# Kernel tuning notes

Measured on AMD Instinct MI355X. Metric: run time of the kernel, lower is better.

## Reference

```python
import jax, jax.numpy as jnp
import numpy as np

NT = 32          # nt_states
T = 64           # t_states
ST = NT + T      # total states
NEG = -1e9       # matches self.huge fill


def setup_inputs() -> dict:
    key = jax.random.key(0)
    k1, k2, k3 = jax.random.split(key, 3)
    B, n = 8, 28
    return {
        "unary_scores": jax.random.normal(k1, (B, n, T), dtype=jnp.float32),
        "rule_scores": jax.random.normal(k2, (B, NT, ST, ST), dtype=jnp.float32),
        "root_scores": jax.random.normal(k3, (B, NT), dtype=jnp.float32),
    }


def _inside(unary_scores, rule_scores, root_scores):
    # Chart indexed beta[b, width, start, state]; span (s, s+w) lives at [b, w, s].
    # Invalid (state-range) slots hold NEG, so exp() underflows them to exactly 0,
    # reproducing the terminal/nonterminal slice logic of the torch code.
    B, n, _ = unary_scores.shape
    beta = jnp.full((B, n, n, ST), NEG, dtype=unary_scores.dtype)
    beta = beta.at[:, 0, :, NT:].set(unary_scores)  # width-0 diagonal: preterminals

    mrule = rule_scores.max(axis=(2, 3))                    # [B, A]
    erule = jnp.exp(rule_scores - mrule[:, :, None, None])  # [B, A, L, R]

    for w in range(1, n):
        S = n - w                     # number of valid start positions
        k = np.arange(w)              # split offset: u = s + k
        # left child: span (s, s+k) -> width k, start s
        left = beta[:, :w, :S, :]                                  # [B, w, S, ST]
        # right child: span (s+k+1, s+w) -> width w-1-k, start s+k+1
        sr = k[:, None] + 1 + np.arange(S)[None, :]                # [w, S]
        right = beta[:, (w - 1 - k)[:, None], sr, :]               # [B, w, S, ST]

        # stable logsumexp over (k, l, r) via exp-space matmuls
        ml = left.max(-1)                                          # [B, w, S]
        mr = right.max(-1)                                         # [B, w, S]
        M = (ml + mr).max(1)                                       # [B, S]
        el = jnp.exp(left - ml[..., None])
        er = jnp.exp(right - mr[..., None] + (ml + mr - M[:, None, :])[..., None])
        numer = jnp.einsum('bksl,bksr->bslr', el, er)              # [B, S, L, R]
        total = jnp.einsum('bslr,balr->bsa', numer, erule)         # [B, S, A]
        score = jnp.log(total) + M[..., None] + mrule[:, None, :]
        beta = beta.at[:, w, :S, :NT].set(score)

    top = beta[:, n - 1, 0, :NT] + root_scores                     # span (0, n-1)
    return jax.nn.logsumexp(top, axis=1)                           # log Z, [B]


def reference(unary_scores, rule_scores, root_scores):
    return _inside(unary_scores, rule_scores, root_scores)
```

## Files before the change

kernel.cpp:

```cpp
#include <hip/hip_runtime.h>
#include <cstdint>
#include <cstddef>


#define NMAX 28
#define SLOT 17344
#define MROW 17280
#define MPROW 17312

#define O_BW1 0
#define O_BMX 960
#define O_G   1744
#define O_MSP 2528
#define O_EMR 2560
#define O_NUM 2592
#define O_RED 6160
#define O_ELT 20496
#define O_ELK 6160
#define O_ERK 14480
#define O_TRI 22800
#define LDSF  34864

__device__ __forceinline__ int off32(int w, int n) {
    return (w - 1) * n - (w * (w - 1)) / 2;
}
__device__ __forceinline__ float gload(const float* p) {
    return __hip_atomic_load(p, __ATOMIC_RELAXED, __HIP_MEMORY_SCOPE_AGENT);
}
__device__ __forceinline__ void gstore(float* p, float v) {
    __hip_atomic_store(p, v, __ATOMIC_RELAXED, __HIP_MEMORY_SCOPE_AGENT);
}
__device__ __forceinline__ unsigned gloadu(const unsigned* p) {
    return __hip_atomic_load(p, __ATOMIC_RELAXED, __HIP_MEMORY_SCOPE_AGENT);
}
__device__ __forceinline__ void gstoreu(unsigned* p, unsigned v) {
    __hip_atomic_store(p, v, __ATOMIC_RELAXED, __HIP_MEMORY_SCOPE_AGENT);
}
__device__ __forceinline__ float dot4acc(float4 m, float4 t, float acc) {
    return fmaf(m.x, t.x, fmaf(m.y, t.y, fmaf(m.z, t.z, fmaf(m.w, t.w, acc))));
}

__global__ __launch_bounds__(256) void mrule_kernel(const float* __restrict__ rule,
                                                    float* __restrict__ mrule,
                                                    unsigned* __restrict__ flags) {
    int a = blockIdx.x, b = blockIdx.y, tid = threadIdx.x;
    if (a == 0 && tid < 32)
        gstoreu(&flags[b * 32 + tid], (tid >= 16 && tid < 20) ? 2u : 0u);
    const float* base = rule + (size_t)(b * 32 + a) * 9216;
    float v = -3.0e38f;
    for (int i = tid; i < 9216; i += 256) v = fmaxf(v, base[i]);
    for (int off = 32; off > 0; off >>= 1) v = fmaxf(v, __shfl_xor(v, off, 64));
    __shared__ float red[4];
    if ((tid & 63) == 0) red[tid >> 6] = v;
    __syncthreads();
    if (tid == 0)
        mrule[b * 32 + a] = fmaxf(fmaxf(red[0], red[1]), fmaxf(red[2], red[3]));
}

__global__ __launch_bounds__(256) void pack_kernel(const float* __restrict__ rule,
                                                   const float* __restrict__ mrule,
                                                   float* __restrict__ E_TT,
                                                   float* __restrict__ E_TN,
                                                   float* __restrict__ E_NT,
                                                   float* __restrict__ E_NN) {
    int b = blockIdx.y, tid = threadIdx.x;
    int a = tid & 31;
    int cc = blockIdx.x * 8 + (tid >> 5);
    float mr = mrule[b * 32 + a];
    int l, r;
    float* dst;
    if (cc < 1024) {
        int flat = cc * 4;
        l = 32 + (flat >> 6); r = 32 + (flat & 63);
        dst = E_TT + ((size_t)(b * 1024 + cc) * 32 + a) * 4;
    } else if (cc < 1536) {
        int flat = (cc - 1024) * 4;
        l = 32 + (flat >> 5); r = flat & 31;
        dst = E_TN + ((size_t)(b * 512 + (cc - 1024)) * 32 + a) * 4;
    } else if (cc < 2048) {
        int flat = (cc - 1536) * 4;
        l = flat >> 6; r = 32 + (flat & 63);
        dst = E_NT + ((size_t)(b * 512 + (cc - 1536)) * 32 + a) * 4;
    } else {
        int flat = (cc - 2048) * 4;
        l = flat >> 5; r = flat & 31;
        dst = E_NN + ((size_t)(b * 256 + (cc - 2048)) * 32 + a) * 4;
    }
    const float4 v = *(const float4*)(rule + (((size_t)(b * 32 + a) * 96 + l) * 96 + r));
    float4 o;
    o.x = expf(v.x - mr); o.y = expf(v.y - mr);
    o.z = expf(v.z - mr); o.w = expf(v.w - mr);
    *(float4*)dst = o;
}

__device__ __forceinline__ void spin_flags(const unsigned* f, unsigned tgt, int tid) {
    if (tid < 64) {
        for (;;) {
            unsigned v = (tid < 20) ? gloadu(&f[tid]) : tgt;
            if (__ballot(v < tgt) == 0ull) break;
            __builtin_amdgcn_s_sleep(2);
        }
    }
    __syncthreads();
}

__global__ __launch_bounds__(1024, 4) void inside_kernel(
    const float* __restrict__ unary, const float* __restrict__ mrule,
    const float* __restrict__ E_TT, const float* __restrict__ E_TN,
    const float* __restrict__ E_NT, const float* __restrict__ E_NN,
    float* __restrict__ part, const float* __restrict__ root,
    float* __restrict__ out, unsigned* __restrict__ flags, int n) {
    extern __shared__ float lds[];
    const int b = blockIdx.x / 20, ch = blockIdx.x % 20;
    const int tid = threadIdx.x;
    const int a = tid & 31;
    unsigned* const myflags = flags + b * 32;
    float* const pbase = part + (size_t)(b * 4) * SLOT;

    float4 e4[2];
    {
        const float4* Eq;
        int base4;
        if (ch < 16) { Eq = (const float4*)E_TT + (size_t)b * 32768; base4 = ch * 64; }
        else         { Eq = (const float4*)E_NN + (size_t)b * 8192;  base4 = (ch - 16) * 64; }
        #pragma unroll
        for (int i = 0; i < 2; ++i)
            e4[i] = Eq[(size_t)(base4 + (tid >> 5) * 2 + i) * 32 + a];
    }
    if (tid < 32) lds[O_EMR + tid] = __expf(mrule[b * 32 + tid]);
    for (int pos = tid >> 6; pos < n; pos += 16) {
        int t = tid & 63;
        float v = unary[((size_t)b * n + pos) * 64 + t];
        float m = v;
        for (int off = 32; off > 0; off >>= 1) m = fmaxf(m, __shfl_xor(m, off, 64));
        if (t == 0) lds[O_BMX + pos] = m;
        if (ch < 16) lds[O_ELT + t * 29 + pos] = __expf(v - m);
    }
    __syncthreads();

    if (ch < 16) {
        for (int w = 1; w < n; ++w) {
            const int S = n - w;
            float* pbW = pbase + (size_t)(w & 3) * SLOT;

            if (w >= 2) {
                spin_flags(myflags, (unsigned)(w - 1), tid);
                const int wp = w - 1;
                const float* pbP = pbase + (size_t)(wp & 3) * SLOT;
                if (tid < (S + 1) * 32) {
                    int s = tid >> 5, aa = tid & 31;
                    float q[20];
                    #pragma unroll
                    for (int c = 0; c < 20; ++c) q[c] = gload(&pbP[c * 864 + tid]);
                    float tT = (((q[0] + q[1]) + (q[2] + q[3])) + ((q[4] + q[5]) + (q[6] + q[7])))
                             + (((q[8] + q[9]) + (q[10] + q[11])) + ((q[12] + q[13]) + (q[14] + q[15])));
                    float t = tT;
                    if (wp >= 3) {
                        float tN = (q[16] + q[17]) + (q[18] + q[19]);
                        float Mp = gload(&pbP[MPROW + s]);
                        t = fmaf(__expf(Mp - lds[O_MSP + s]), tN, tT);
                    }
                    float t2 = t * lds[O_EMR + aa];
                    float m2 = t2;
                    for (int off = 16; off > 0; off >>= 1)
                        m2 = fmaxf(m2, __shfl_xor(m2, off, 32));
                    lds[O_BW1 + aa * 30 + s] = t2 / m2;
                    if (aa == 0)
                        lds[O_BMX + wp * NMAX + s] = __logf(m2) + lds[O_MSP + s];
                }
                __syncthreads();
            }

            if (tid < S) {
                int s = tid;
                float M = -3.0e38f;
                for (int k = 0; k < w; ++k)
                    M = fmaxf(M, lds[O_BMX + k * NMAX + s] +
                                  lds[O_BMX + (w - 1 - k) * NMAX + s + k + 1]);
                lds[O_MSP + s] = M;
                lds[O_G + s] =
                    __expf(lds[O_BMX + s] + lds[O_BMX + (w - 1) * NMAX + s + 1] - M);
                lds[O_G + NMAX + s] =
                    __expf(lds[O_BMX + (w - 1) * NMAX + s] + lds[O_BMX + s + w] - M);
                if (ch == 0) gstore(&pbW[MROW + s], M);
            }
            __syncthreads();

            {
                const int cL = tid & 255, sh = tid >> 8;
                const bool tn = (w >= 2) && (ch < 8);
                const int cc = (w == 1) ? ch * 256 + cL
                             : (ch < 8 ? ch * 256 + cL : (ch - 8) * 256 + cL);
                int l, r;
                if (tn) { l = cc >> 5; r = cc & 31; }
                else    { l = cc >> 6; r = cc & 63; }
                unsigned short* np = (unsigned short*)(lds + O_NUM);
                for (int s = sh; s < S; s += 4) {
                    float v;
                    if (w == 1)
                        v = lds[O_ELT + l * 29 + s] * lds[O_ELT + r * 29 + (s + 1)] *
                            lds[O_G + s];
                    else if (tn)
                        v = lds[O_ELT + l * 29 + s] * lds[O_BW1 + r * 30 + (s + 1)] *
                            lds[O_G + s];
                    else
                        v = lds[O_BW1 + l * 30 + s] * lds[O_ELT + r * 29 + (s + w)] *
                            lds[O_G + NMAX + s];
                    unsigned u = __float_as_uint(v);
                    np[s * 264 + cL] = (unsigned short)((u + 0x7fffu + ((u >> 16) & 1u)) >> 16);
                }
            }
            __syncthreads();

            {
                const char* nbase = (const char*)(lds + O_NUM);
                const int g32 = tid >> 5, wv = tid >> 6;
                const bool lowhalf = (tid & 32) == 0;
                for (int s = 0; s < S; ++s) {
                    uint4 u = *(const uint4*)(nbase + s * 528 + g32 * 16);
                    float acc = 0.f;
                    #define LO(q) __uint_as_float((q) << 16)
                    #define HI(q) __uint_as_float((q) & 0xffff0000u)
                    acc = fmaf(LO(u.x), e4[0].x, acc); acc = fmaf(HI(u.x), e4[0].y, acc);
                    acc = fmaf(LO(u.y), e4[0].z, acc); acc = fmaf(HI(u.y), e4[0].w, acc);
                    acc = fmaf(LO(u.z), e4[1].x, acc); acc = fmaf(HI(u.z), e4[1].y, acc);
                    acc = fmaf(LO(u.w), e4[1].z, acc); acc = fmaf(HI(u.w), e4[1].w, acc);
                    #undef LO
                    #undef HI
                    acc += __shfl_xor(acc, 32, 64);
                    if (lowhalf) lds[O_RED + wv * 896 + s * 32 + a] = acc;
                }
            }
            __syncthreads();

            if (tid < S * 32) {
                float t = 0.f;
                #pragma unroll
                for (int g2 = 0; g2 < 16; ++g2) t += lds[O_RED + g2 * 896 + tid];
                gstore(&pbW[ch * 864 + tid], t);
            }
            __syncthreads();
            if (tid == 0) gstoreu(&myflags[ch], (unsigned)w);

            if (w == 1) {
                const float4* Eq = (ch < 8)
                    ? (const float4*)E_TN + (size_t)b * 16384 + (size_t)(ch * 64) * 32
                    : (const float4*)E_NT + (size_t)b * 16384 + (size_t)((ch - 8) * 64) * 32;
                #pragma unroll
                for (int i = 0; i < 2; ++i)
                    e4[i] = Eq[(size_t)((tid >> 5) * 2 + i) * 32 + a];
            }
        }

        if (ch == 0) {
            spin_flags(myflags, (unsigned)(n - 1), tid);
            if (tid < 32) {
                const float* pbP = pbase + (size_t)((n - 1) & 3) * SLOT;
                float q[20];
                #pragma unroll
                for (int c = 0; c < 20; ++c) q[c] = gload(&pbP[c * 864 + tid]);
                float tT = (((q[0] + q[1]) + (q[2] + q[3])) + ((q[4] + q[5]) + (q[6] + q[7])))
                         + (((q[8] + q[9]) + (q[10] + q[11])) + ((q[12] + q[13]) + (q[14] + q[15])));
                float tN = (q[16] + q[17]) + (q[18] + q[19]);
                float Mp = gload(&pbP[MPROW + 0]);
                float t = fmaf(__expf(Mp - lds[O_MSP + 0]), tN, tT);
                float v = __logf(t) + lds[O_MSP + 0] + mrule[b * 32 + tid] + root[b * 32 + tid];
                float m = v;
                for (int off = 16; off > 0; off >>= 1) m = fmaxf(m, __shfl_xor(m, off, 32));
                float e = __expf(v - m);
                for (int off = 16; off > 0; off >>= 1) e += __shfl_xor(e, off, 32);
                if (tid == 0) out[b] = m + __logf(e);
            }
        }
    } else {
        for (int w = 3; w < n; ++w) {
            const int S = n - w, Sp2 = S | 1;
            int q4 = (w - 2 + 3) >> 2; if (!(q4 & 1)) ++q4;
            const int K4 = 4 * q4;
            float* pbW = pbase + (size_t)(w & 3) * SLOT;

            spin_flags(myflags, (unsigned)(w - 2), tid);

            {
                const int wf = w - 2;
                const float* pbF = pbase + (size_t)(wf & 3) * SLOT;
                if (tid < (n - wf) * 32) {
                    int s = tid >> 5, aa = tid & 31;
                    float q[20];
                    #pragma unroll
                    for (int c = 0; c < 20; ++c) q[c] = gload(&pbF[c * 864 + tid]);
                    float tT = (((q[0] + q[1]) + (q[2] + q[3])) + ((q[4] + q[5]) + (q[6] + q[7])))
                             + (((q[8] + q[9]) + (q[10] + q[11])) + ((q[12] + q[13]) + (q[14] + q[15])));
                    float Mf = gload(&pbF[MROW + s]);
                    float t = tT;
                    if (wf >= 3) {
                        float tN = (q[16] + q[17]) + (q[18] + q[19]);
                        float Mp = gload(&pbF[MPROW + s]);
                        t = fmaf(__expf(Mp - Mf), tN, tT);
                    }
                    float t2 = t * lds[O_EMR + aa];
                    float m2 = t2;
                    for (int off = 16; off > 0; off >>= 1)
                        m2 = fmaxf(m2, __shfl_xor(m2, off, 32));
                    lds[O_TRI + (off32(wf, n) + s) * 32 + aa] = t2 / m2;
                    if (aa == 0) lds[O_BMX + wf * NMAX + s] = __logf(m2) + Mf;
                }
                __syncthreads();
            }

            if (tid < (w - 2) * 32) {
                int k = (tid >> 5) + 1, s = tid & 31;
                if (s < S) {
                    float Mp = -3.0e38f;
                    for (int k2 = 1; k2 <= w - 2; ++k2)
                        Mp = fmaxf(Mp, lds[O_BMX + k2 * NMAX + s] +
                                       lds[O_BMX + (w - 1 - k2) * NMAX + s + k2 + 1]);
                    lds[O_G + k * NMAX + s] =
                        __expf(lds[O_BMX + k * NMAX + s] +
                               lds[O_BMX + (w - 1 - k) * NMAX + s + k + 1] - Mp);
                    if (k == 1 && ch == 16) gstore(&pbW[MPROW + s], Mp);
                }
            }
            __syncthreads();

            if (tid < S * 32) {
                int s = tid >> 5, sym = tid & 31;
                int off = (sym * Sp2 + s) * K4;
                for (int kk = 1; kk <= w - 2; ++kk) {
                    lds[O_ELK + off + kk - 1] =
                        lds[O_TRI + (off32(kk, n) + s) * 32 + sym];
                    lds[O_ERK + off + kk - 1] =
                        lds[O_TRI + (off32(w - 1 - kk, n) + s + kk + 1) * 32 + sym] *
                        lds[O_G + kk * NMAX + s];
                }
                for (int k = w - 2; k < K4; ++k) {
                    lds[O_ELK + off + k] = 0.f;
                    lds[O_ERK + off + k] = 0.f;
                }
            }
            __syncthreads();

            {
                const int cL = tid & 255, sh = tid >> 8;
                const int cc = (ch - 16) * 256 + cL;
                const int l = cc >> 5, r = cc & 31;
                unsigned short* np = (unsigned short*)(lds + O_NUM);
                for (int s = sh; s < S; s += 4) {
                    const float* elp = lds + O_ELK + (l * Sp2 + s) * K4;
                    const float* erp = lds + O_ERK + (r * Sp2 + s) * K4;
                    float acc = 0.f;
                    for (int j = 0; j < K4; j += 4)
                        acc = dot4acc(*(const float4*)(elp + j),
                                      *(const float4*)(erp + j), acc);
                    unsigned u = __float_as_uint(acc);
                    np[s * 264 + cL] = (unsigned short)((u + 0x7fffu + ((u >> 16) & 1u)) >> 16);
                }
            }
            __syncthreads();

            {
                const char* nbase = (const char*)(lds + O_NUM);
                const int g32 = tid >> 5, wv = tid >> 6;
                const bool lowhalf = (tid & 32) == 0;
                for (int s = 0; s < S; ++s) {
                    uint4 u = *(const uint4*)(nbase + s * 528 + g32 * 16);
                    float acc = 0.f;
                    #define LO(q) __uint_as_float((q) << 16)
                    #define HI(q) __uint_as_float((q) & 0xffff0000u)
                    acc = fmaf(LO(u.x), e4[0].x, acc); acc = fmaf(HI(u.x), e4[0].y, acc);
                    acc = fmaf(LO(u.y), e4[0].z, acc); acc = fmaf(HI(u.y), e4[0].w, acc);
                    acc = fmaf(LO(u.z), e4[1].x, acc); acc = fmaf(HI(u.z), e4[1].y, acc);
                    acc = fmaf(LO(u.w), e4[1].z, acc); acc = fmaf(HI(u.w), e4[1].w, acc);
                    #undef LO
                    #undef HI
                    acc += __shfl_xor(acc, 32, 64);
                    if (lowhalf) lds[O_RED + wv * 896 + s * 32 + a] = acc;
                }
            }
            __syncthreads();

            if (tid < S * 32) {
                float t = 0.f;
                #pragma unroll
                for (int g2 = 0; g2 < 16; ++g2) t += lds[O_RED + g2 * 896 + tid];
                gstore(&pbW[ch * 864 + tid], t);
            }
            __syncthreads();
            if (tid == 0) gstoreu(&myflags[ch], (unsigned)w);
        }
    }
}

extern "C" void kernel_launch(void* const* d_in, const int* in_sizes, int n_in,
                              void* d_out, int out_size, void* d_ws, size_t ws_size,
                              hipStream_t stream) {
    const float* unary = (const float*)d_in[0];
    const float* rule  = (const float*)d_in[1];
    const float* root  = (const float*)d_in[2];
    float* out = (float*)d_out;

    const int B = in_sizes[2] / 32;
    int n = in_sizes[0] / (B * 64);

    float* ws = (float*)d_ws;
    float* mrule  = ws;
    float* E_TT   = mrule + (size_t)B * 32;
    float* E_TN   = E_TT + (size_t)B * 131072;
    float* E_NT   = E_TN + (size_t)B * 65536;
    float* E_NN   = E_NT + (size_t)B * 65536;
    float* part   = E_NN + (size_t)B * 32768;
    unsigned* flags = (unsigned*)(part + (size_t)B * 4 * SLOT);

    mrule_kernel<<<dim3(32, B), 256, 0, stream>>>(rule, mrule, flags);
    pack_kernel<<<dim3(288, B), 256, 0, stream>>>(rule, mrule, E_TT, E_TN, E_NT, E_NN);

    hipFuncSetAttribute((const void*)inside_kernel,
                        hipFuncAttributeMaxDynamicSharedMemorySize, LDSF * 4);

    void* args[] = {
        (void*)&unary, (void*)&mrule,
        (void*)&E_TT, (void*)&E_TN, (void*)&E_NT, (void*)&E_NN,
        (void*)&part, (void*)&root, (void*)&out, (void*)&flags, (void*)&n
    };
    hipLaunchCooperativeKernel((void*)inside_kernel, dim3(B * 20), dim3(1024),
                               args, LDSF * 4, stream);
}
```

Baseline: 242.7 us.

## Replace flag-based sync with sign-encoded data polling and fewer, wider blocks

Removes the per-chunk flag array and spin-wait barrier. Consumers now poll the partial-sum slots directly, and readiness is encoded by sign-flipping the values on alternating slot reuse, with slots pre-initialised to a negative sentinel. Per-batch blocks drop from 20 to 12, so each block covers twice the rule chunk. Partials are laid out with a 12-float pitch per (s,a) and the max values are recomputed locally instead of exchanged through global memory. This aims to cut flag round-trip latency and synchronisation cost, at the price of more work per block and correctness that relies on the sign encoding holding.

```diff
diff --git a/kernel.cpp b/kernel.cpp
--- a/kernel.cpp
+++ b/kernel.cpp
@@ -4,9 +4,8 @@
 
 
 #define NMAX 28
-#define SLOT 17344
-#define MROW 17280
-#define MPROW 17312
+#define PITCH 12
+#define SLOTF 10368
 
 #define O_BW1 0
 #define O_BMX 960
@@ -14,12 +13,12 @@
 #define O_MSP 2528
 #define O_EMR 2560
 #define O_NUM 2592
-#define O_RED 6160
-#define O_ELT 20496
-#define O_ELK 6160
-#define O_ERK 14480
-#define O_TRI 22800
-#define LDSF  34864
+#define O_RED 9612
+#define O_ELT 23948
+#define O_ELK 9612
+#define O_ERK 17932
+#define O_TRI 26252
+#define LDSF  38316
 
 __device__ __forceinline__ int off32(int w, int n) {
     return (w - 1) * n - (w * (w - 1)) / 2;
@@ -30,22 +29,13 @@
 __device__ __forceinline__ void gstore(float* p, float v) {
     __hip_atomic_store(p, v, __ATOMIC_RELAXED, __HIP_MEMORY_SCOPE_AGENT);
 }
-__device__ __forceinline__ unsigned gloadu(const unsigned* p) {
-    return __hip_atomic_load(p, __ATOMIC_RELAXED, __HIP_MEMORY_SCOPE_AGENT);
-}
-__device__ __forceinline__ void gstoreu(unsigned* p, unsigned v) {
-    __hip_atomic_store(p, v, __ATOMIC_RELAXED, __HIP_MEMORY_SCOPE_AGENT);
-}
 __device__ __forceinline__ float dot4acc(float4 m, float4 t, float acc) {
     return fmaf(m.x, t.x, fmaf(m.y, t.y, fmaf(m.z, t.z, fmaf(m.w, t.w, acc))));
 }
 
 __global__ __launch_bounds__(256) void mrule_kernel(const float* __restrict__ rule,
-                                                    float* __restrict__ mrule,
-                                                    unsigned* __restrict__ flags) {
+                                                    float* __restrict__ mrule) {
     int a = blockIdx.x, b = blockIdx.y, tid = threadIdx.x;
-    if (a == 0 && tid < 32)
-        gstoreu(&flags[b * 32 + tid], (tid >= 16 && tid < 20) ? 2u : 0u);
     const float* base = rule + (size_t)(b * 32 + a) * 9216;
     float v = -3.0e38f;
     for (int i = tid; i < 9216; i += 256) v = fmaxf(v, base[i]);
@@ -62,8 +52,14 @@
                                                    float* __restrict__ E_TT,
                                                    float* __restrict__ E_TN,
                                                    float* __restrict__ E_NT,
-                                                   float* __restrict__ E_NN) {
+                                                   float* __restrict__ E_NN,
+                                                   float* __restrict__ part) {
     int b = blockIdx.y, tid = threadIdx.x;
+    {
+        const int total = 4 * SLOTF;
+        for (int i = blockIdx.x * 256 + tid; i < total; i += 288 * 256)
+            part[(size_t)b * total + i] = -0.5f;
+    }
     int a = tid & 31;
     int cc = blockIdx.x * 8 + (tid >> 5);
     float mr = mrule[b * 32 + a];
@@ -93,15 +89,22 @@
     *(float4*)dst = o;
 }
 
-__device__ __forceinline__ void spin_flags(const unsigned* f, unsigned tgt, int tid) {
-    if (tid < 64) {
-        for (;;) {
-            unsigned v = (tid < 20) ? gloadu(&f[tid]) : tgt;
-            if (__ballot(v < tgt) == 0ull) break;
-            __builtin_amdgcn_s_sleep(2);
+__device__ __forceinline__ void poll12(const float* pp, bool oddp, int CHp,
+                                       float x[12]) {
+    for (;;) {
+        #pragma unroll
+        for (int c = 0; c < 12; ++c) x[c] = gload(pp + c);
+        if (oddp) {
+            #pragma unroll
+            for (int c = 0; c < 12; ++c) x[c] = -x[c] - 1.0f;
         }
-    }
-    __syncthreads();
+        float mn = fminf(fminf(fminf(x[0], x[1]), fminf(x[2], x[3])),
+                         fminf(fminf(x[4], x[5]), fminf(x[6], x[7])));
+        if (CHp == 12)
+            mn = fminf(mn, fminf(fminf(x[8], x[9]), fminf(x[10], x[11])));
+        if (mn >= 0.0f) break;
+        __builtin_amdgcn_s_sleep(4);
+    }
 }
 
 __global__ __launch_bounds__(1024, 4) void inside_kernel(
@@ -109,23 +112,24 @@
     const float* __restrict__ E_TT, const float* __restrict__ E_TN,
     const float* __restrict__ E_NT, const float* __restrict__ E_NN,
     float* __restrict__ part, const float* __restrict__ root,
-    float* __restrict__ out, unsigned* __restrict__ flags, int n) {
+    float* __restrict__ out, int n) {
     extern __shared__ float lds[];
-    const int b = blockIdx.x / 20, ch = blockIdx.x % 20;
+    const int b = blockIdx.x / 12, ch = blockIdx.x % 12;
     const int tid = threadIdx.x;
-    const int a = tid & 31;
-    unsigned* const myflags = flags + b * 32;
-    float* const pbase = part + (size_t)(b * 4) * SLOT;
-
-    float4 e4[2];
-    {
-        const float4* Eq;
-        int base4;
-        if (ch < 16) { Eq = (const float4*)E_TT + (size_t)b * 32768; base4 = ch * 64; }
-        else         { Eq = (const float4*)E_NN + (size_t)b * 8192;  base4 = (ch - 16) * 64; }
+    const int a = tid & 31, g = tid >> 5;
+    float* const pbase = part + (size_t)(b * 4) * SLOTF;
+
+    float4 e4[4];
+    if (ch < 8) {
+        const float4* Eq = (const float4*)E_TT + (size_t)b * 32768;
+        #pragma unroll
+        for (int i = 0; i < 4; ++i)
+            e4[i] = Eq[(size_t)(ch * 128 + g * 4 + i) * 32 + a];
+    } else {
+        const float4* Eq = (const float4*)E_NN + (size_t)b * 8192;
         #pragma unroll
         for (int i = 0; i < 2; ++i)
-            e4[i] = Eq[(size_t)(base4 + (tid >> 5) * 2 + i) * 32 + a];
+            e4[i] = Eq[(size_t)((ch - 8) * 64 + g * 2 + i) * 32 + a];
     }
     if (tid < 32) lds[O_EMR + tid] = __expf(mrule[b * 32 + tid]);
     for (int pos = tid >> 6; pos < n; pos += 16) {
@@ -134,30 +138,34 @@
         float m = v;
         for (int off = 32; off > 0; off >>= 1) m = fmaxf(m, __shfl_xor(m, off, 64));
         if (t == 0) lds[O_BMX + pos] = m;
-        if (ch < 16) lds[O_ELT + t * 29 + pos] = __expf(v - m);
+        if (ch < 8) lds[O_ELT + t * 29 + pos] = __expf(v - m);
     }
     __syncthreads();
 
-    if (ch < 16) {
+    if (ch < 8) {
         for (int w = 1; w < n; ++w) {
             const int S = n - w;
-            float* pbW = pbase + (size_t)(w & 3) * SLOT;
+            const bool oddw = ((w >> 2) & 1) != 0;
+            float* pbW = pbase + (size_t)(w & 3) * SLOTF;
 
             if (w >= 2) {
-                spin_flags(myflags, (unsigned)(w - 1), tid);
                 const int wp = w - 1;
-                const float* pbP = pbase + (size_t)(wp & 3) * SLOT;
+                const int CHp = (wp >= 3) ? 12 : 8;
+                const bool oddp = ((wp >> 2) & 1) != 0;
+                const float* pbP = pbase + (size_t)(wp & 3) * SLOTF;
                 if (tid < (S + 1) * 32) {
                     int s = tid >> 5, aa = tid & 31;
-                    float q[20];
-                    #pragma unroll
-                    for (int c = 0; c < 20; ++c) q[c] = gload(&pbP[c * 864 + tid]);
-                    float tT = (((q[0] + q[1]) + (q[2] + q[3])) + ((q[4] + q[5]) + (q[6] + q[7])))
-                             + (((q[8] + q[9]) + (q[10] + q[11])) + ((q[12] + q[13]) + (q[14] + q[15])));
+                    float Mp = -3.0e38f;
+                    for (int k = 1; k <= wp - 2; ++k)
+                        Mp = fmaxf(Mp, lds[O_BMX + k * NMAX + s] +
+                                       lds[O_BMX + (wp - 1 - k) * NMAX + s + k + 1]);
+                    float x[12];
+                    poll12(pbP + (size_t)tid * PITCH, oddp, CHp, x);
+                    float tT = (((x[0] + x[1]) + (x[2] + x[3])) +
+                                ((x[4] + x[5]) + (x[6] + x[7])));
                     float t = tT;
-                    if (wp >= 3) {
-                        float tN = (q[16] + q[17]) + (q[18] + q[19]);
-                        float Mp = gload(&pbP[MPROW + s]);
+                    if (CHp == 12) {
+                        float tN = (x[8] + x[9]) + (x[10] + x[11]);
                         t = fmaf(__expf(Mp - lds[O_MSP + s]), tN, tT);
                     }
                     float t2 = t * lds[O_EMR + aa];
@@ -168,8 +176,8 @@
                     if (aa == 0)
                         lds[O_BMX + wp * NMAX + s] = __logf(m2) + lds[O_MSP + s];
                 }
-                __syncthreads();
-            }
+            }
+            __syncthreads();
 
             if (tid < S) {
                 int s = tid;
@@ -182,20 +190,19 @@
                     __expf(lds[O_BMX + s] + lds[O_BMX + (w - 1) * NMAX + s + 1] - M);
                 lds[O_G + NMAX + s] =
                     __expf(lds[O_BMX + (w - 1) * NMAX + s] + lds[O_BMX + s + w] - M);
-                if (ch == 0) gstore(&pbW[MROW + s], M);
             }
             __syncthreads();
 
             {
-                const int cL = tid & 255, sh = tid >> 8;
-                const bool tn = (w >= 2) && (ch < 8);
-                const int cc = (w == 1) ? ch * 256 + cL
-                             : (ch < 8 ? ch * 256 + cL : (ch - 8) * 256 + cL);
+                const int cL = tid & 511, sh = tid >> 9;
+                const bool tn = (w >= 2) && (ch < 4);
+                const int cc = (w == 1) ? ch * 512 + cL
+                             : (ch < 4 ? ch * 512 + cL : (ch - 4) * 512 + cL);
                 int l, r;
                 if (tn) { l = cc >> 5; r = cc & 31; }
                 else    { l = cc >> 6; r = cc & 63; }
                 unsigned short* np = (unsigned short*)(lds + O_NUM);
-                for (int s = sh; s < S; s += 4) {
+                for (int s = sh; s < S; s += 2) {
                     float v;
                     if (w == 1)
                         v = lds[O_ELT + l * 29 + s] * lds[O_ELT + r * 29 + (s + 1)] *
@@ -207,17 +214,172 @@
                         v = lds[O_BW1 + l * 30 + s] * lds[O_ELT + r * 29 + (s + w)] *
                             lds[O_G + NMAX + s];
                     unsigned u = __float_as_uint(v);
-                    np[s * 264 + cL] = (unsigned short)((u + 0x7fffu + ((u >> 16) & 1u)) >> 16);
+                    np[s * 520 + cL] = (unsigned short)((u + 0x7fffu + ((u >> 16) & 1u)) >> 16);
                 }
             }
             __syncthreads();
 
             {
                 const char* nbase = (const char*)(lds + O_NUM);
-                const int g32 = tid >> 5, wv = tid >> 6;
+                const int wv = tid >> 6;
                 const bool lowhalf = (tid & 32) == 0;
                 for (int s = 0; s < S; ++s) {
-                    uint4 u = *(const uint4*)(nbase + s * 528 + g32 * 16);
+                    uint4 u0 = *(const uint4*)(nbase + s * 1040 + g * 32);
+                    uint4 u1 = *(const uint4*)(nbase + s * 1040 + g * 32 + 16);
+                    float acc = 0.f;
+                    #define LO(q) __uint_as_float((q) << 16)
+                    #define HI(q) __uint_as_float((q) & 0xffff0000u)
+                    acc = fmaf(LO(u0.x), e4[0].x, acc); acc = fmaf(HI(u0.x), e4[0].y, acc);
+                    acc = fmaf(LO(u0.y), e4[0].z, acc); acc = fmaf(HI(u0.y), e4[0].w, acc);
+                    acc = fmaf(LO(u0.z), e4[1].x, acc); acc = fmaf(HI(u0.z), e4[1].y, acc);
+                    acc = fmaf(LO(u0.w), e4[1].z, acc); acc = fmaf(HI(u0.w), e4[1].w, acc);
+                    acc = fmaf(LO(u1.x), e4[2].x, acc); acc = fmaf(HI(u1.x), e4[2].y, acc);
+                    acc = fmaf(LO(u1.y), e4[2].z, acc); acc = fmaf(HI(u1.y), e4[2].w, acc);
+                    acc = fmaf(LO(u1.z), e4[3].x, acc); acc = fmaf(HI(u1.z), e4[3].y, acc);
+                    acc = fmaf(LO(u1.w), e4[3].z, acc); acc = fmaf(HI(u1.w), e4[3].w, acc);
+                    #undef LO
+                    #undef HI
+                    acc += __shfl_xor(acc, 32, 64);
+                    if (lowhalf) lds[O_RED + wv * 896 + s * 32 + a] = acc;
+                }
+            }
+            __syncthreads();
+
+            if (tid < S * 32) {
+                float t = 0.f;
+                #pragma unroll
+                for (int g2 = 0; g2 < 16; ++g2) t += lds[O_RED + g2 * 896 + tid];
+                gstore(&pbW[(size_t)tid * PITCH + ch], oddw ? (-t - 1.0f) : t);
+            }
+
+            if (w == 1) {
+                const float4* Eq = (ch < 4)
+                    ? (const float4*)E_TN + (size_t)b * 16384 + (size_t)(ch * 128) * 32
+                    : (const float4*)E_NT + (size_t)b * 16384 + (size_t)((ch - 4) * 128) * 32;
+                #pragma unroll
+                for (int i = 0; i < 4; ++i)
+                    e4[i] = Eq[(size_t)(g * 4 + i) * 32 + a];
+            }
+        }
+
+        if (ch == 0 && tid < 32) {
+            const int wp = n - 1;
+            const bool oddp = ((wp >> 2) & 1) != 0;
+            const float* pbP = pbase + (size_t)(wp & 3) * SLOTF;
+            float Mp = -3.0e38f;
+            for (int k = 1; k <= wp - 2; ++k)
+                Mp = fmaxf(Mp, lds[O_BMX + k * NMAX + 0] +
+                               lds[O_BMX + (wp - 1 - k) * NMAX + k + 1]);
+            float x[12];
+            poll12(pbP + (size_t)tid * PITCH, oddp, 12, x);
+            float tT = (((x[0] + x[1]) + (x[2] + x[3])) +
+                        ((x[4] + x[5]) + (x[6] + x[7])));
+            float tN = (x[8] + x[9]) + (x[10] + x[11]);
+            float t = fmaf(__expf(Mp - lds[O_MSP + 0]), tN, tT);
+            float v = __logf(t) + lds[O_MSP + 0] + mrule[b * 32 + tid] + root[b * 32 + tid];
+            float m = v;
+            for (int off = 16; off > 0; off >>= 1) m = fmaxf(m, __shfl_xor(m, off, 32));
+            float e = __expf(v - m);
+            for (int off = 16; off > 0; off >>= 1) e += __shfl_xor(e, off, 32);
+            if (tid == 0) out[b] = m + __logf(e);
+        }
+    } else {
+        for (int w = 3; w < n; ++w) {
+            const int S = n - w, Sp2 = S | 1;
+            int q4 = (w - 2 + 3) >> 2; if (!(q4 & 1)) ++q4;
+            const int K4 = 4 * q4;
+            const bool oddw = ((w >> 2) & 1) != 0;
+            float* pbW = pbase + (size_t)(w & 3) * SLOTF;
+
+            {
+                const int wf = w - 2;
+                const int CHp = (wf >= 3) ? 12 : 8;
+                const bool oddp = ((wf >> 2) & 1) != 0;
+                const float* pbF = pbase + (size_t)(wf & 3) * SLOTF;
+                if (tid < (n - wf) * 32) {
+                    int s = tid >> 5, aa = tid & 31;
+                    float Mw = -3.0e38f;
+                    for (int k = 0; k < wf; ++k)
+                        Mw = fmaxf(Mw, lds[O_BMX + k * NMAX + s] +
+                                       lds[O_BMX + (wf - 1 - k) * NMAX + s + k + 1]);
+                    float Mp = -3.0e38f;
+                    for (int k = 1; k <= wf - 2; ++k)
+                        Mp = fmaxf(Mp, lds[O_BMX + k * NMAX + s] +
+                                       lds[O_BMX + (wf - 1 - k) * NMAX + s + k + 1]);
+                    float x[12];
+                    poll12(pbF + (size_t)tid * PITCH, oddp, CHp, x);
+                    float tT = (((x[0] + x[1]) + (x[2] + x[3])) +
+                                ((x[4] + x[5]) + (x[6] + x[7])));
+                    float t = tT;
+                    if (CHp == 12) {
+                        float tN = (x[8] + x[9]) + (x[10] + x[11]);
+                        t = fmaf(__expf(Mp - Mw), tN, tT);
+                    }
+                    float t2 = t * lds[O_EMR + aa];
+                    float m2 = t2;
+                    for (int off = 16; off > 0; off >>= 1)
+                        m2 = fmaxf(m2, __shfl_xor(m2, off, 32));
+                    lds[O_TRI + (off32(wf, n) + s) * 32 + aa] = t2 / m2;
+                    if (aa == 0) lds[O_BMX + wf * NMAX + s] = __logf(m2) + Mw;
+                }
+            }
+            __syncthreads();
+
+            if (tid < (w - 2) * 32) {
+                int k = (tid >> 5) + 1, s = tid & 31;
+                if (s < S) {
+                    float Mp = -3.0e38f;
+                    for (int k2 = 1; k2 <= w - 2; ++k2)
+                        Mp = fmaxf(Mp, lds[O_BMX + k2 * NMAX + s] +
+                                       lds[O_BMX + (w - 1 - k2) * NMAX + s + k2 + 1]);
+                    lds[O_G + k * NMAX + s] =
+                        __expf(lds[O_BMX + k * NMAX + s] +
+                               lds[O_BMX + (w - 1 - k) * NMAX + s + k + 1] - Mp);
+                }
+            }
+            __syncthreads();
+
+            if (tid < S * 32) {
+                int s = tid >> 5, sym = tid & 31;
+                int off = (sym * Sp2 + s) * K4;
+                for (int kk = 1; kk <= w - 2; ++kk) {
+                    lds[O_ELK + off + kk - 1] =
+                        lds[O_TRI + (off32(kk, n) + s) * 32 + sym];
+                    lds[O_ERK + off + kk - 1] =
+                        lds[O_TRI + (off32(w - 1 - kk, n) + s + kk + 1) * 32 + sym] *
+                        lds[O_G + kk * NMAX + s];
+                }
+                for (int k = w - 2; k < K4; ++k) {
+                    lds[O_ELK + off + k] = 0.f;
+                    lds[O_ERK + off + k] = 0.f;
+                }
+            }
+            __syncthreads();
+
+            {
+                const int cL = tid & 255, sh = tid >> 8;
+                const int cc = (ch - 8) * 256 + cL;
+                const int l = cc >> 5, r = cc & 31;
+                unsigned short* np = (unsigned short*)(lds + O_NUM);
+                for (int s = sh; s < S; s += 4) {
+                    const float* elp = lds + O_ELK + (l * Sp2 + s) * K4;
+                    const float* erp = lds + O_ERK + (r * Sp2 + s) * K4;
+                    float acc = 0.f;
+                    for (int j = 0; j < K4; j += 4)
+                        acc = dot4acc(*(const float4*)(elp + j),
+                                      *(const float4*)(erp + j), acc);
+                    unsigned u = __float_as_uint(acc);
+                    np[s * 520 + cL] = (unsigned short)((u + 0x7fffu + ((u >> 16) & 1u)) >> 16);
+                }
+            }
+            __syncthreads();
+
+            {
+                const char* nbase = (const char*)(lds + O_NUM);
+                const int wv = tid >> 6;
+                const bool lowhalf = (tid & 32) == 0;
+                for (int s = 0; s < S; ++s) {
+                    uint4 u = *(const uint4*)(nbase + s * 1040 + g * 16);
                     float acc = 0.f;
                     #define LO(q) __uint_as_float((q) << 16)
                     #define HI(q) __uint_as_float((q) & 0xffff0000u)
@@ -237,156 +399,9 @@
                 float t = 0.f;
                 #pragma unroll
                 for (int g2 = 0; g2 < 16; ++g2) t += lds[O_RED + g2 * 896 + tid];
-                gstore(&pbW[ch * 864 + tid], t);
-            }
-            __syncthreads();
-            if (tid == 0) gstoreu(&myflags[ch], (unsigned)w);
-
-            if (w == 1) {
-                const float4* Eq = (ch < 8)
-                    ? (const float4*)E_TN + (size_t)b * 16384 + (size_t)(ch * 64) * 32
-                    : (const float4*)E_NT + (size_t)b * 16384 + (size_t)((ch - 8) * 64) * 32;
-                #pragma unroll
-                for (int i = 0; i < 2; ++i)
-                    e4[i] = Eq[(size_t)((tid >> 5) * 2 + i) * 32 + a];
-            }
-        }
-
-        if (ch == 0) {
-            spin_flags(myflags, (unsigned)(n - 1), tid);
-            if (tid < 32) {
-                const float* pbP = pbase + (size_t)((n - 1) & 3) * SLOT;
-                float q[20];
-                #pragma unroll
-                for (int c = 0; c < 20; ++c) q[c] = gload(&pbP[c * 864 + tid]);
-                float tT = (((q[0] + q[1]) + (q[2] + q[3])) + ((q[4] + q[5]) + (q[6] + q[7])))
-                         + (((q[8] + q[9]) + (q[10] + q[11])) + ((q[12] + q[13]) + (q[14] + q[15])));
-                float tN = (q[16] + q[17]) + (q[18] + q[19]);
-                float Mp = gload(&pbP[MPROW + 0]);
-                float t = fmaf(__expf(Mp - lds[O_MSP + 0]), tN, tT);
-                float v = __logf(t) + lds[O_MSP + 0] + mrule[b * 32 + tid] + root[b * 32 + tid];
-                float m = v;
-                for (int off = 16; off > 0; off >>= 1) m = fmaxf(m, __shfl_xor(m, off, 32));
-                float e = __expf(v - m);
-                for (int off = 16; off > 0; off >>= 1) e += __shfl_xor(e, off, 32);
-                if (tid == 0) out[b] = m + __logf(e);
-            }
-        }
-    } else {
-        for (int w = 3; w < n; ++w) {
-            const int S = n - w, Sp2 = S | 1;
-            int q4 = (w - 2 + 3) >> 2; if (!(q4 & 1)) ++q4;
-            const int K4 = 4 * q4;
-            float* pbW = pbase + (size_t)(w & 3) * SLOT;
-
-            spin_flags(myflags, (unsigned)(w - 2), tid);
-
-            {
-                const int wf = w - 2;
-                const float* pbF = pbase + (size_t)(wf & 3) * SLOT;
-                if (tid < (n - wf) * 32) {
-                    int s = tid >> 5, aa = tid & 31;
-                    float q[20];
-                    #pragma unroll
-                    for (int c = 0; c < 20; ++c) q[c] = gload(&pbF[c * 864 + tid]);
-                    float tT = (((q[0] + q[1]) + (q[2] + q[3])) + ((q[4] + q[5]) + (q[6] + q[7])))
-                             + (((q[8] + q[9]) + (q[10] + q[11])) + ((q[12] + q[13]) + (q[14] + q[15])));
-                    float Mf = gload(&pbF[MROW + s]);
-                    float t = tT;
-                    if (wf >= 3) {
-                        float tN = (q[16] + q[17]) + (q[18] + q[19]);
-                        float Mp = gload(&pbF[MPROW + s]);
-                        t = fmaf(__expf(Mp - Mf), tN, tT);
-                    }
-                    float t2 = t * lds[O_EMR + aa];
-                    float m2 = t2;
-                    for (int off = 16; off > 0; off >>= 1)
-                        m2 = fmaxf(m2, __shfl_xor(m2, off, 32));
-                    lds[O_TRI + (off32(wf, n) + s) * 32 + aa] = t2 / m2;
-                    if (aa == 0) lds[O_BMX + wf * NMAX + s] = __logf(m2) + Mf;
-                }
-                __syncthreads();
-            }
-
-            if (tid < (w - 2) * 32) {
-                int k = (tid >> 5) + 1, s = tid & 31;
-                if (s < S) {
-                    float Mp = -3.0e38f;
-                    for (int k2 = 1; k2 <= w - 2; ++k2)
-                        Mp = fmaxf(Mp, lds[O_BMX + k2 * NMAX + s] +
-                                       lds[O_BMX + (w - 1 - k2) * NMAX + s + k2 + 1]);
-                    lds[O_G + k * NMAX + s] =
-                        __expf(lds[O_BMX + k * NMAX + s] +
-                               lds[O_BMX + (w - 1 - k) * NMAX + s + k + 1] - Mp);
-                    if (k == 1 && ch == 16) gstore(&pbW[MPROW + s], Mp);
-                }
-            }
-            __syncthreads();
-
-            if (tid < S * 32) {
-                int s = tid >> 5, sym = tid & 31;
-                int off = (sym * Sp2 + s) * K4;
-                for (int kk = 1; kk <= w - 2; ++kk) {
-                    lds[O_ELK + off + kk - 1] =
-                        lds[O_TRI + (off32(kk, n) + s) * 32 + sym];
-                    lds[O_ERK + off + kk - 1] =
-                        lds[O_TRI + (off32(w - 1 - kk, n) + s + kk + 1) * 32 + sym] *
-                        lds[O_G + kk * NMAX + s];
-                }
-                for (int k = w - 2; k < K4; ++k) {
-                    lds[O_ELK + off + k] = 0.f;
-                    lds[O_ERK + off + k] = 0.f;
-                }
-            }
-            __syncthreads();
-
-            {
-                const int cL = tid & 255, sh = tid >> 8;
-                const int cc = (ch - 16) * 256 + cL;
-                const int l = cc >> 5, r = cc & 31;
-                unsigned short* np = (unsigned short*)(lds + O_NUM);
-                for (int s = sh; s < S; s += 4) {
-                    const float* elp = lds + O_ELK + (l * Sp2 + s) * K4;
-                    const float* erp = lds + O_ERK + (r * Sp2 + s) * K4;
-                    float acc = 0.f;
-                    for (int j = 0; j < K4; j += 4)
-                        acc = dot4acc(*(const float4*)(elp + j),
-                                      *(const float4*)(erp + j), acc);
-                    unsigned u = __float_as_uint(acc);
-                    np[s * 264 + cL] = (unsigned short)((u + 0x7fffu + ((u >> 16) & 1u)) >> 16);
-                }
-            }
-            __syncthreads();
-
-            {
-                const char* nbase = (const char*)(lds + O_NUM);
-                const int g32 = tid >> 5, wv = tid >> 6;
-                const bool lowhalf = (tid & 32) == 0;
-                for (int s = 0; s < S; ++s) {
-                    uint4 u = *(const uint4*)(nbase + s * 528 + g32 * 16);
-                    float acc = 0.f;
-                    #define LO(q) __uint_as_float((q) << 16)
-                    #define HI(q) __uint_as_float((q) & 0xffff0000u)
-                    acc = fmaf(LO(u.x), e4[0].x, acc); acc = fmaf(HI(u.x), e4[0].y, acc);
-                    acc = fmaf(LO(u.y), e4[0].z, acc); acc = fmaf(HI(u.y), e4[0].w, acc);
-                    acc = fmaf(LO(u.z), e4[1].x, acc); acc = fmaf(HI(u.z), e4[1].y, acc);
-                    acc = fmaf(LO(u.w), e4[1].z, acc); acc = fmaf(HI(u.w), e4[1].w, acc);
-                    #undef LO
-                    #undef HI
-                    acc += __shfl_xor(acc, 32, 64);
-                    if (lowhalf) lds[O_RED + wv * 896 + s * 32 + a] = acc;
-                }
-            }
-            __syncthreads();
-
-            if (tid < S * 32) {
-                float t = 0.f;
-                #pragma unroll
-                for (int g2 = 0; g2 < 16; ++g2) t += lds[O_RED + g2 * 896 + tid];
-                gstore(&pbW[ch * 864 + tid], t);
-            }
-            __syncthreads();
-            if (tid == 0) gstoreu(&myflags[ch], (unsigned)w);
+                gstore(&pbW[(size_t)tid * PITCH + ch], oddw ? (-t - 1.0f) : t);
+            }
+            __syncthreads();
         }
     }
 }
@@ -409,10 +424,10 @@
     float* E_NT   = E_TN + (size_t)B * 65536;
     float* E_NN   = E_NT + (size_t)B * 65536;
     float* part   = E_NN + (size_t)B * 32768;
-    unsigned* flags = (unsigned*)(part + (size_t)B * 4 * SLOT);
-
-    mrule_kernel<<<dim3(32, B), 256, 0, stream>>>(rule, mrule, flags);
-    pack_kernel<<<dim3(288, B), 256, 0, stream>>>(rule, mrule, E_TT, E_TN, E_NT, E_NN);
+
+    mrule_kernel<<<dim3(32, B), 256, 0, stream>>>(rule, mrule);
+    pack_kernel<<<dim3(288, B), 256, 0, stream>>>(rule, mrule, E_TT, E_TN, E_NT,
+                                                  E_NN, part);
 
     hipFuncSetAttribute((const void*)inside_kernel,
                         hipFuncAttributeMaxDynamicSharedMemorySize, LDSF * 4);
@@ -420,8 +435,8 @@
     void* args[] = {
         (void*)&unary, (void*)&mrule,
         (void*)&E_TT, (void*)&E_TN, (void*)&E_NT, (void*)&E_NN,
-        (void*)&part, (void*)&root, (void*)&out, (void*)&flags, (void*)&n
+        (void*)&part, (void*)&root, (void*)&out, (void*)&n
     };
-    hipLaunchCooperativeKernel((void*)inside_kernel, dim3(B * 20), dim3(1024),
+    hipLaunchCooperativeKernel((void*)inside_kernel, dim3(B * 12), dim3(1024),
                                args, LDSF * 4, stream);
 }
```

Measured after the change: 315.6 us. 30.0% more time.
